# Performance work log

Measured on AMD Instinct MI355X. Metric: run time of the kernel, lower is better.

## Reference

```python
import jax, jax.numpy as jnp
import numpy as np

N_HEAD = 12
D_HEAD = 64


def setup_inputs() -> dict:
    key = jax.random.key(0)
    ks = jax.random.split(key, 9)
    bs, seq, d_model = 4, 2048, 768
    sc = 1.0 / np.sqrt(d_model)
    return {
        "q": jax.random.normal(ks[0], (bs, seq, d_model), jnp.float32),
        "k": jax.random.normal(ks[1], (bs, seq, d_model), jnp.float32),
        "v": jax.random.normal(ks[2], (bs, seq, d_model), jnp.float32),
        "Wq": jax.random.normal(ks[3], (d_model, d_model), jnp.float32) * sc,
        "bq": jax.random.normal(ks[4], (d_model,), jnp.float32) * 0.01,
        "Wk": jax.random.normal(ks[5], (d_model, d_model), jnp.float32) * sc,
        "bk": jax.random.normal(ks[6], (d_model,), jnp.float32) * 0.01,
        "Wv": jax.random.normal(ks[7], (d_model, d_model), jnp.float32) * sc,
        "bv": jax.random.normal(ks[8], (d_model,), jnp.float32) * 0.01,
    }


def _split_heads(x):
    # [bs, seq, n_head*d_head] -> [bs, n_head, seq, d_head]
    bs, seq, _ = x.shape
    return x.reshape(bs, seq, N_HEAD, D_HEAD).transpose(0, 2, 1, 3)


def reference(q, k, v, Wq, bq, Wk, bk, Wv, bv):
    # Linear projections (torch Linear: x @ W.T + b)
    wq = _split_heads(q @ Wq.T + bq)
    wk = _split_heads(k @ Wk.T + bk)
    wv = _split_heads(v @ Wv.T + bv)
    # scale=False in defaults -> raw dot products, no mask, dropout is eval no-op
    scores = jnp.einsum("bhqd,bhkd->bhqk", wq, wk)  # [bs, h, S, S]
    probs = jax.nn.softmax(scores, axis=-1)
    attn_vec = jnp.einsum("bhqk,bhkd->bhqd", probs, wv)
    bs, _, seq, _ = attn_vec.shape
    # merge heads -> [bs, seq, n_head*d_head]
    return attn_vec.transpose(0, 2, 1, 3).reshape(bs, seq, N_HEAD * D_HEAD)
```

## Files before the change

kernel.cpp:

```cpp
#include <hip/hip_runtime.h>
#include <stdint.h>

typedef _Float16 half8  __attribute__((ext_vector_type(8)));
typedef _Float16 half4v __attribute__((ext_vector_type(4)));
typedef float    floatx4 __attribute__((ext_vector_type(4)));

#define LOG2E 1.44269504088896340736f

__device__ __forceinline__ void gl_lds16(const _Float16* g, _Float16* l) {
  __builtin_amdgcn_global_load_lds(
      (__attribute__((address_space(1))) void*)g,
      (__attribute__((address_space(3))) void*)l, 16, 0, 0);
}
__device__ __forceinline__ void gl_lds16f(const float* g, float* l) {
  __builtin_amdgcn_global_load_lds(
      (__attribute__((address_space(1))) void*)g,
      (__attribute__((address_space(3))) void*)l, 16, 0, 0);
}

__device__ __forceinline__ half4v pack4(float a, float b, float c, float d) {
  auto lo = __builtin_amdgcn_cvt_pkrtz(a, b);
  auto hi = __builtin_amdgcn_cvt_pkrtz(c, d);
  return half4v{static_cast<_Float16>(lo[0]), static_cast<_Float16>(lo[1]),
                static_cast<_Float16>(hi[0]), static_cast<_Float16>(hi[1])};
}
__device__ __forceinline__ half8 cvt8(floatx4 a, floatx4 b) {
  half4v lo = pack4(a[0], a[1], a[2], a[3]);
  half4v hi = pack4(b[0], b[1], b[2], b[3]);
  return __builtin_shufflevector(lo, hi, 0, 1, 2, 3, 4, 5, 6, 7);
}

struct CvtArgs {
  const float* src[3];
  _Float16*    dst[3];
};

__global__ void cvt_kernel(CvtArgs a) {
  const int z = blockIdx.y;
  const int i = (blockIdx.x * 256 + threadIdx.x) * 8;
  const float4* s = (const float4*)(a.src[z] + i);
  float4 v0 = s[0], v1 = s[1];
  half8 h = { (_Float16)v0.x, (_Float16)v0.y, (_Float16)v0.z, (_Float16)v0.w,
              (_Float16)v1.x, (_Float16)v1.y, (_Float16)v1.z, (_Float16)v1.w };
  *(half8*)(a.dst[z] + i) = h;
}


__device__ __forceinline__ void gemm_stage(const float* __restrict__ X,
                                           const _Float16* __restrict__ W,
                                           float* Asb, _Float16* Bsb,
                                           int m0, int n0, int k0, int tid) {
  #pragma unroll
  for (int i = 0; i < 4; ++i) {
    int G = i * 256 + tid;
    int r = G >> 3, gl = G & 7;
    int g = gl ^ (r & 7);
    gl_lds16f(X + (size_t)(m0 + r) * 768 + k0 + g * 4, Asb + G * 4);
  }
  #pragma unroll
  for (int i = 0; i < 2; ++i) {
    int G = i * 256 + tid;
    int r = G >> 2, gl = G & 3;
    int g = gl ^ ((r >> 1) & 3);
    gl_lds16(W + (size_t)(n0 + r) * 768 + k0 + g * 8, Bsb + G * 8);
  }
}

template <int BUF>
__device__ __forceinline__ void gemm_body(
    int knext, const float* __restrict__ X, const _Float16* __restrict__ W,
    float* As, _Float16* Bs, int m0, int n0, int tid, int z,
    int wr, int wc, int qd, int col, floatx4 (&acc)[4][4])
{
  if (knext < 768)
    gemm_stage(X, W, As + (1 - BUF) * 4096, Bs + (1 - BUF) * 4096, m0, n0, knext, tid);

  half8 af[4], bf[4];
  #pragma unroll
  for (int t = 0; t < 4; ++t) {
    int ra = wr * 64 + t * 16 + col;
    const float* Ab = As + BUF * 4096 + ra * 32;
    floatx4 a0 = *(const floatx4*)(Ab + (((2 * qd)     ^ (ra & 7)) * 4));
    floatx4 a1 = *(const floatx4*)(Ab + (((2 * qd + 1) ^ (ra & 7)) * 4));
    af[t] = cvt8(a0, a1);
  }
  #pragma unroll
  for (int t = 0; t < 4; ++t) {
    int rb = wc * 64 + t * 16 + col;
    bf[t] = *(const half8*)(Bs + BUF * 4096 + rb * 32 + ((qd ^ ((rb >> 1) & 3)) * 8));
  }
  if (z == 2) {
    #pragma unroll
    for (int i = 0; i < 4; ++i)
      #pragma unroll
      for (int j = 0; j < 4; ++j)
        acc[i][j] = __builtin_amdgcn_mfma_f32_16x16x32_f16(af[i], bf[j], acc[i][j], 0, 0, 0);
  } else {
    #pragma unroll
    for (int i = 0; i < 4; ++i)
      #pragma unroll
      for (int j = 0; j < 4; ++j)
        acc[i][j] = __builtin_amdgcn_mfma_f32_16x16x32_f16(bf[j], af[i], acc[i][j], 0, 0, 0);
  }
  __syncthreads();
}

__global__ __launch_bounds__(256, 2) void qkv_gemm(
    const float* __restrict__ qx, const float* __restrict__ kx, const float* __restrict__ vx,
    const _Float16* __restrict__ wh,
    const float* __restrict__ bqp, const float* __restrict__ bkp, const float* __restrict__ bvp,
    _Float16* __restrict__ oq, _Float16* __restrict__ ok, _Float16* __restrict__ ovt)
{
  __shared__ __attribute__((aligned(16))) float    As[2 * 4096];
  __shared__ __attribute__((aligned(16))) _Float16 Bs[2 * 4096];
  const int z  = blockIdx.z;
  const float* X = (z == 0) ? qx : ((z == 1) ? kx : vx);
  const _Float16* W = wh + (size_t)z * 589824;
  const int m0 = blockIdx.x * 128, n0 = blockIdx.y * 128;
  const int tid  = threadIdx.x;
  const int lane = tid & 63, wid = tid >> 6;
  const int wr = wid >> 1, wc = wid & 1;
  const int qd = lane >> 4, col = lane & 15;

  const floatx4 z4 = {0.f, 0.f, 0.f, 0.f};
  floatx4 acc[4][4];
  #pragma unroll
  for (int i = 0; i < 4; ++i)
    #pragma unroll
    for (int j = 0; j < 4; ++j) acc[i][j] = z4;

  gemm_stage(X, W, As, Bs, m0, n0, 0, tid);
  __syncthreads();
  for (int kk = 0; kk < 768; kk += 64) {
    gemm_body<0>(kk + 32, X, W, As, Bs, m0, n0, tid, z, wr, wc, qd, col, acc);
    gemm_body<1>(kk + 64, X, W, As, Bs, m0, n0, tid, z, wr, wc, qd, col, acc);
  }

  const float* bias = (z == 0) ? bqp : ((z == 1) ? bkp : bvp);
  if (z == 2) {
    #pragma unroll
    for (int j = 0; j < 4; ++j) {
      int n = n0 + wc * 64 + j * 16 + col;
      float bb = bias[n];
      #pragma unroll
      for (int i = 0; i < 4; ++i) {
        int m = m0 + wr * 64 + i * 16 + qd * 4;
        int b = m >> 11, s = m & 2047;
        half4v h;
        #pragma unroll
        for (int r = 0; r < 4; ++r) h[r] = (_Float16)(acc[i][j][r] + bb);
        *(half4v*)(ovt + ((size_t)(b * 768 + n)) * 2048 + s) = h;
      }
    }
  } else {
    _Float16* O = (z == 0) ? oq : ok;
    const float scale = (z == 0) ? LOG2E : 1.0f;
    #pragma unroll
    for (int j = 0; j < 4; ++j) {
      int n = n0 + wc * 64 + j * 16 + qd * 4;
      float4 bb = *(const float4*)(bias + n);
      int hh = n >> 6, d = n & 63;
      #pragma unroll
      for (int i = 0; i < 4; ++i) {
        int m = m0 + wr * 64 + i * 16 + col;
        int b = m >> 11, s = m & 2047;
        half4v h;
        h[0] = (_Float16)((acc[i][j][0] + bb.x) * scale);
        h[1] = (_Float16)((acc[i][j][1] + bb.y) * scale);
        h[2] = (_Float16)((acc[i][j][2] + bb.z) * scale);
        h[3] = (_Float16)((acc[i][j][3] + bb.w) * scale);
        *(half4v*)(O + (size_t)(b * 12 + hh) * 131072 + (size_t)s * 64 + d) = h;
      }
    }
  }
}


__device__ __forceinline__ void stage_kv(const _Float16* __restrict__ Kg,
                                         const _Float16* __restrict__ Vg,
                                         _Float16* ksd, _Float16* vsd, int j0, int tid) {
  #pragma unroll
  for (int i = 0; i < 2; ++i) {
    int c = i * 256 + tid;
    int row = c >> 3, sc = c & 7;
    gl_lds16(Kg + (size_t)(j0 + row) * 64 + ((sc ^ (row & 7)) * 8), ksd + c * 8);
    gl_lds16(Vg + (size_t)row * 2048 + j0 + ((sc ^ (row & 7)) * 8), vsd + c * 8);
  }
}

template <int BUF>
__device__ __forceinline__ void attn_body(
    int jnext, const _Float16* __restrict__ Kg, const _Float16* __restrict__ Vg,
    _Float16* Ks, _Float16* Vs, int tid,
    const half8 (&qf)[2][2], int kb0, int kb1, const int (&vb)[4],
    floatx4 (&negm)[2], floatx4 (&ol)[2], floatx4 (&o)[4][2])
{
  if (jnext < 2048)
    stage_kv(Kg, Vg, Ks + (1 - BUF) * 4096, Vs + (1 - BUF) * 4096, jnext, tid);

  const char* ksb = (const char*)Ks;
  const char* vsb = (const char*)Vs;

  floatx4 st[4][2];
  #pragma unroll
  for (int t = 0; t < 4; ++t) {
    half8 kf0 = *(const half8*)(ksb + BUF * 8192 + t * 2048 + kb0);
    half8 kf1 = *(const half8*)(ksb + BUF * 8192 + t * 2048 + kb1);
    #pragma unroll
    for (int qt = 0; qt < 2; ++qt) {
      st[t][qt] = __builtin_amdgcn_mfma_f32_16x16x32_f16(kf0, qf[qt][0], negm[qt], 0, 0, 0);
      st[t][qt] = __builtin_amdgcn_mfma_f32_16x16x32_f16(kf1, qf[qt][1], st[t][qt], 0, 0, 0);
    }
  }

  float mr[2];
  #pragma unroll
  for (int qt = 0; qt < 2; ++qt) {
    float v = fmaxf(
        fmaxf(fmaxf(fmaxf(st[0][qt][0], st[0][qt][1]), fmaxf(st[0][qt][2], st[0][qt][3])),
              fmaxf(fmaxf(st[1][qt][0], st[1][qt][1]), fmaxf(st[1][qt][2], st[1][qt][3]))),
        fmaxf(fmaxf(fmaxf(st[2][qt][0], st[2][qt][1]), fmaxf(st[2][qt][2], st[2][qt][3])),
              fmaxf(fmaxf(st[3][qt][0], st[3][qt][1]), fmaxf(st[3][qt][2], st[3][qt][3]))));
    v = fmaxf(v, __shfl_xor(v, 16, 64));
    v = fmaxf(v, __shfl_xor(v, 32, 64));
    mr[qt] = fmaxf(v, 0.f);
  }

  half4v pf[4][2];
  #pragma unroll
  for (int qt = 0; qt < 2; ++qt)
    #pragma unroll
    for (int t = 0; t < 4; ++t)
      pf[t][qt] = pack4(__builtin_amdgcn_exp2f(st[t][qt][0] - mr[qt]),
                        __builtin_amdgcn_exp2f(st[t][qt][1] - mr[qt]),
                        __builtin_amdgcn_exp2f(st[t][qt][2] - mr[qt]),
                        __builtin_amdgcn_exp2f(st[t][qt][3] - mr[qt]));

  if (__any(mr[0] > 0.f || mr[1] > 0.f)) {
    #pragma unroll
    for (int qt = 0; qt < 2; ++qt) {
      float al = __builtin_amdgcn_exp2f(-mr[qt]);
      negm[qt] -= mr[qt];
      ol[qt] *= al;
      #pragma unroll
      for (int dt = 0; dt < 4; ++dt) o[dt][qt] *= al;
    }
  }

  const half4v vone = {(_Float16)1.0f, (_Float16)1.0f, (_Float16)1.0f, (_Float16)1.0f};
  #pragma unroll
  for (int dt = 0; dt < 4; ++dt) {
    #pragma unroll
    for (int t = 0; t < 4; ++t) {
      half4v vf = *(const half4v*)(vsb + BUF * 8192 + dt * 2048 + vb[t]);
      #pragma unroll
      for (int qt = 0; qt < 2; ++qt)
        o[dt][qt] = __builtin_amdgcn_mfma_f32_16x16x16f16(vf, pf[t][qt], o[dt][qt], 0, 0, 0);
    }
  }
  #pragma unroll
  for (int t = 0; t < 4; ++t)
    #pragma unroll
    for (int qt = 0; qt < 2; ++qt)
      ol[qt] = __builtin_amdgcn_mfma_f32_16x16x16f16(vone, pf[t][qt], ol[qt], 0, 0, 0);

  __syncthreads();
}

__global__ __launch_bounds__(256, 3) void attn_kernel(
    const _Float16* __restrict__ Qm,
    const _Float16* __restrict__ Km,
    const _Float16* __restrict__ Vt,
    float* __restrict__ out)
{
  __shared__ __attribute__((aligned(16))) _Float16 Ks[2 * 4096];
  __shared__ __attribute__((aligned(16))) _Float16 Vs[2 * 4096];
  const int bh = blockIdx.y;
  const int q0 = blockIdx.x * 128;
  const int tid = threadIdx.x, lane = tid & 63, w = tid >> 6;
  const int qd = lane >> 4, col = lane & 15, c7 = col & 7;
  const _Float16* Qg = Qm + (size_t)bh * 131072;
  const _Float16* Kg = Km + (size_t)bh * 131072;
  const _Float16* Vg = Vt + (size_t)bh * 131072;

  half8 qf[2][2];
  #pragma unroll
  for (int qt = 0; qt < 2; ++qt)
    #pragma unroll
    for (int ks = 0; ks < 2; ++ks)
      qf[qt][ks] = *(const half8*)(Qg + (size_t)(q0 + w * 32 + qt * 16 + col) * 64
                                   + (ks * 4 + qd) * 8);

  const int kb0 = col * 128 + ((qd ^ c7) * 16);
  const int kb1 = col * 128 + (((4 + qd) ^ c7) * 16);
  const int vq = (qd >> 1) ^ c7;
  int vb[4];
  #pragma unroll
  for (int t = 0; t < 4; ++t)
    vb[t] = col * 128 + (qd & 1) * 8 + ((vq ^ (2 * t)) * 16);

  floatx4 negm[2] = {{100.f, 100.f, 100.f, 100.f}, {100.f, 100.f, 100.f, 100.f}};
  const floatx4 z4 = {0.f, 0.f, 0.f, 0.f};
  floatx4 ol[2] = {z4, z4};
  floatx4 o[4][2];
  #pragma unroll
  for (int dt = 0; dt < 4; ++dt)
    #pragma unroll
    for (int qt = 0; qt < 2; ++qt) o[dt][qt] = z4;

  stage_kv(Kg, Vg, Ks, Vs, 0, tid);
  __syncthreads();

  for (int jj = 0; jj < 2048; jj += 128) {
    attn_body<0>(jj + 64,  Kg, Vg, Ks, Vs, tid, qf, kb0, kb1, vb, negm, ol, o);
    attn_body<1>(jj + 128, Kg, Vg, Ks, Vs, tid, qf, kb0, kb1, vb, negm, ol, o);
  }

  const int b = bh / 12, h = bh % 12;
  #pragma unroll
  for (int qt = 0; qt < 2; ++qt) {
    float inv = 1.0f / ol[qt][0];
    int qg = q0 + w * 32 + qt * 16 + col;
    float* obase = out + ((size_t)b * 2048 + qg) * 768 + h * 64;
    #pragma unroll
    for (int dt = 0; dt < 4; ++dt) {
      floatx4 v = o[dt][qt];
      v *= inv;
      *(floatx4*)(obase + dt * 16 + qd * 4) = v;
    }
  }
}

extern "C" void kernel_launch(void* const* d_in, const int* in_sizes, int n_in,
                              void* d_out, int out_size, void* d_ws, size_t ws_size,
                              hipStream_t stream) {
  const float* q  = (const float*)d_in[0];
  const float* k  = (const float*)d_in[1];
  const float* v  = (const float*)d_in[2];
  const float* Wq = (const float*)d_in[3];
  const float* bq = (const float*)d_in[4];
  const float* Wk = (const float*)d_in[5];
  const float* bk = (const float*)d_in[6];
  const float* Wv = (const float*)d_in[7];
  const float* bv = (const float*)d_in[8];

  const size_t NX = 6291456;
  const size_t NW = 589824;
  const size_t need = (3 * NW + 3 * NX) * sizeof(_Float16);
  if (ws_size < need) return;

  _Float16* wh = (_Float16*)d_ws;
  _Float16* qh = wh + 3 * NW;
  _Float16* kh = qh + NX;
  _Float16* vt = kh + NX;

  CvtArgs ca;
  ca.src[0] = Wq; ca.src[1] = Wk; ca.src[2] = Wv;
  ca.dst[0] = wh; ca.dst[1] = wh + NW; ca.dst[2] = wh + 2 * NW;

  cvt_kernel<<<dim3(288, 3), 256, 0, stream>>>(ca);
  qkv_gemm<<<dim3(64, 6, 3), 256, 0, stream>>>(q, k, v, wh, bq, bk, bv, qh, kh, vt);
  attn_kernel<<<dim3(16, 48), 256, 0, stream>>>(qh, kh, vt, (float*)d_out);
}
```

Measured before the change: 267.9 us.

## Stage QKV GEMM epilogue through LDS for coalesced 16-byte stores; swap attention grid order

The QKV projection epilogue now writes the bias-added fp16 tile into shared memory, which reuses the GEMM staging buffers, and then reads it back so each thread can issue contiguous 16-byte global stores. Before, the epilogue used scattered 8-byte stores, including transposed V writes. The attention grid is also transposed so that consecutive blocks cover different batch-heads rather than different query tiles of the same head, which changes the launch order and how K/V reuse is spread across the GPU. The staging adds a barrier and extra LDS traffic to the epilogue.

```diff
diff --git a/kernel.cpp b/kernel.cpp
--- a/kernel.cpp
+++ b/kernel.cpp
@@ -111,8 +111,11 @@
     const float* __restrict__ bqp, const float* __restrict__ bkp, const float* __restrict__ bvp,
     _Float16* __restrict__ oq, _Float16* __restrict__ ok, _Float16* __restrict__ ovt)
 {
-  __shared__ __attribute__((aligned(16))) float    As[2 * 4096];
-  __shared__ __attribute__((aligned(16))) _Float16 Bs[2 * 4096];
+  __shared__ __attribute__((aligned(16))) char smem[49152];
+  float*    As = (float*)smem;
+  _Float16* Bs = (_Float16*)(smem + 32768);
+  _Float16* Es = (_Float16*)smem;
+
   const int z  = blockIdx.z;
   const float* X = (z == 0) ? qx : ((z == 1) ? kx : vx);
   const _Float16* W = wh + (size_t)z * 589824;
@@ -137,40 +140,54 @@
   }
 
   const float* bias = (z == 0) ? bqp : ((z == 1) ? bkp : bvp);
+  const int b = m0 >> 11, s0 = m0 & 2047;
   if (z == 2) {
     #pragma unroll
     for (int j = 0; j < 4; ++j) {
-      int n = n0 + wc * 64 + j * 16 + col;
-      float bb = bias[n];
+      int n_loc = wc * 64 + j * 16 + col;
+      float bb = bias[n0 + n_loc];
       #pragma unroll
       for (int i = 0; i < 4; ++i) {
-        int m = m0 + wr * 64 + i * 16 + qd * 4;
-        int b = m >> 11, s = m & 2047;
-        half4v h;
-        #pragma unroll
-        for (int r = 0; r < 4; ++r) h[r] = (_Float16)(acc[i][j][r] + bb);
-        *(half4v*)(ovt + ((size_t)(b * 768 + n)) * 2048 + s) = h;
+        int s_loc = wr * 64 + i * 16 + qd * 4;
+        half4v h = pack4(acc[i][j][0] + bb, acc[i][j][1] + bb,
+                         acc[i][j][2] + bb, acc[i][j][3] + bb);
+        *(half4v*)(Es + n_loc * 160 + s_loc) = h;
       }
+    }
+    __syncthreads();
+    #pragma unroll
+    for (int it = 0; it < 8; ++it) {
+      int row = it * 16 + (tid >> 4);
+      int k   = tid & 15;
+      half8 vr = *(const half8*)(Es + row * 160 + k * 8);
+      *(half8*)(ovt + ((size_t)(b * 768 + n0 + row)) * 2048 + s0 + k * 8) = vr;
     }
   } else {
     _Float16* O = (z == 0) ? oq : ok;
     const float scale = (z == 0) ? LOG2E : 1.0f;
     #pragma unroll
     for (int j = 0; j < 4; ++j) {
-      int n = n0 + wc * 64 + j * 16 + qd * 4;
-      float4 bb = *(const float4*)(bias + n);
-      int hh = n >> 6, d = n & 63;
+      int n_loc = wc * 64 + j * 16 + qd * 4;
+      float4 bb = *(const float4*)(bias + n0 + n_loc);
       #pragma unroll
       for (int i = 0; i < 4; ++i) {
-        int m = m0 + wr * 64 + i * 16 + col;
-        int b = m >> 11, s = m & 2047;
-        half4v h;
-        h[0] = (_Float16)((acc[i][j][0] + bb.x) * scale);
-        h[1] = (_Float16)((acc[i][j][1] + bb.y) * scale);
-        h[2] = (_Float16)((acc[i][j][2] + bb.z) * scale);
-        h[3] = (_Float16)((acc[i][j][3] + bb.w) * scale);
-        *(half4v*)(O + (size_t)(b * 12 + hh) * 131072 + (size_t)s * 64 + d) = h;
+        int s_loc = wr * 64 + i * 16 + col;
+        half4v h = pack4((acc[i][j][0] + bb.x) * scale, (acc[i][j][1] + bb.y) * scale,
+                         (acc[i][j][2] + bb.z) * scale, (acc[i][j][3] + bb.w) * scale);
+        *(half4v*)(Es + s_loc * 160 + n_loc) = h;
       }
+    }
+    __syncthreads();
+    const int hh0 = n0 >> 6;
+    #pragma unroll
+    for (int it = 0; it < 8; ++it) {
+      int seg = it * 32 + (tid >> 3);
+      int s = seg >> 1, hseg = seg & 1;
+      int k = tid & 7;
+      half8 vr = *(const half8*)(Es + s * 160 + hseg * 64 + k * 8);
+      int mb = (m0 + s) >> 11, sg = (m0 + s) & 2047;
+      *(half8*)(O + (size_t)(mb * 12 + hh0 + hseg) * 131072
+                  + (size_t)sg * 64 + k * 8) = vr;
     }
   }
 }
@@ -275,8 +292,8 @@
 {
   __shared__ __attribute__((aligned(16))) _Float16 Ks[2 * 4096];
   __shared__ __attribute__((aligned(16))) _Float16 Vs[2 * 4096];
-  const int bh = blockIdx.y;
-  const int q0 = blockIdx.x * 128;
+  const int bh = blockIdx.x;
+  const int q0 = blockIdx.y * 128;
   const int tid = threadIdx.x, lane = tid & 63, w = tid >> 6;
   const int qd = lane >> 4, col = lane & 15, c7 = col & 7;
   const _Float16* Qg = Qm + (size_t)bh * 131072;
@@ -360,5 +377,5 @@
 
   cvt_kernel<<<dim3(288, 3), 256, 0, stream>>>(ca);
   qkv_gemm<<<dim3(64, 6, 3), 256, 0, stream>>>(q, k, v, wh, bq, bk, bv, qh, kh, vt);
-  attn_kernel<<<dim3(16, 48), 256, 0, stream>>>(qh, kh, vt, (float*)d_out);
-}
+  attn_kernel<<<dim3(48, 16), 256, 0, stream>>>(qh, kh, vt, (float*)d_out);
+}
```

Measured after the change: 254.8 us. 1.05x faster.
